# Kernel tuning notes

Hardware: AMD Instinct MI355X
Metric: run time of the kernel (lower is better)

Reference implementation:

```python
import jax, jax.numpy as jnp
import numpy as np


def setup_inputs() -> dict:
    key = jax.random.key(0)
    ks = jax.random.split(key, 7)
    B, L, D, H = 256, 1024, 768, 768
    x = jax.random.normal(ks[0], (B, L, D), dtype=jnp.float32)
    label_mask = jax.random.randint(ks[1], (B, L), 0, 2).astype(jnp.int32)
    global_prototype_tensor = jax.random.normal(ks[2], (L + 1, D), dtype=jnp.float32)
    W_h = jax.random.normal(ks[3], (H, D), dtype=jnp.float32) * 0.02
    b_h = jax.random.normal(ks[4], (H,), dtype=jnp.float32) * 0.02
    W_p = jax.random.normal(ks[5], (D, H), dtype=jnp.float32) * 0.02
    b_p = jax.random.normal(ks[6], (D,), dtype=jnp.float32) * 0.02
    return {"x": x, "label_mask": label_mask,
            "global_prototype_tensor": global_prototype_tensor,
            "W_h": W_h, "b_h": b_h, "W_p": W_p, "b_p": b_p}


def _mlp(v, W_h, b_h, W_p, b_p):
    # torch Linear: y = v @ W.T + b
    h = jax.nn.relu(jnp.einsum('ld,hd->lh', v, W_h) + b_h)
    return jnp.einsum('lh,dh->ld', h, W_p) + b_p


def reference(x, label_mask, global_prototype_tensor, W_h, b_h, W_p, b_p):
    # x: [B, L, D]; label_mask: [B, L] (1 if label i in example's label_list)
    m = label_mask.astype(x.dtype)                        # [B, L]
    pos_cnt = m.sum(0)                                    # [L]
    B = x.shape[0]
    anti_cnt = B - pos_cnt                                # [L]
    pos_sum = jnp.einsum('bl,bld->ld', m, x)              # masked segment-sum
    tot_sum = x.sum(0)                                    # [L, D]
    anti_sum = tot_sum - pos_sum

    pos_mean = pos_sum / jnp.maximum(pos_cnt, 1.0)[:, None]
    anti_mean = anti_sum / jnp.maximum(anti_cnt, 1.0)[:, None]

    avg_pos = 0.5 * pos_mean + 0.5 * global_prototype_tensor[:-1]   # [L, D]
    avg_anti = 0.5 * anti_mean + 0.5 * global_prototype_tensor[-1]  # [L, D]

    proto = _mlp(avg_pos, W_h, b_h, W_p, b_p)
    proto = jnp.where((pos_cnt > 0)[:, None], proto, 0.0)           # rows stay zero if no members

    anti_proto = _mlp(avg_anti, W_h, b_h, W_p, b_p)
    w = (anti_cnt > 0).astype(x.dtype)                              # [L]
    anti = jnp.einsum('l,ld->d', w, anti_proto) / jnp.maximum(w.sum(), 1.0)

    return jnp.concatenate([proto, anti[None, :]], axis=0)          # [L+1, D]
```

## Files before the change

### kernel.cpp

```cpp
#include <hip/hip_runtime.h>

#define L_DIM 1024
#define B_DIM 256
#define D_DIM 768
#define K_DIM 768
#define NTILES (K_DIM / 32)
#define WN    (768 * 768)

typedef _Float16 half8 __attribute__((ext_vector_type(8)));
typedef float    floatx4 __attribute__((ext_vector_type(4)));

__device__ __forceinline__ ushort f2h(float f) {
    _Float16 h = (_Float16)f;
    return __builtin_bit_cast(ushort, h);
}
__device__ __forceinline__ float h2f(ushort u) {
    return (float)__builtin_bit_cast(_Float16, u);
}

__device__ __forceinline__ void gl16(const ushort* g, ushort* l) {
    __builtin_amdgcn_global_load_lds(
        (const __attribute__((address_space(1))) unsigned int*)g,
        (__attribute__((address_space(3))) unsigned int*)l, 16, 0, 0);
}

__global__ __launch_bounds__(768)
void reduce_and_cast(const float* __restrict__ x,
                     const int* __restrict__ mask,
                     const float* __restrict__ gpt,
                     const float* __restrict__ Wh, const float* __restrict__ Wp,
                     ushort* __restrict__ Vhi, ushort* __restrict__ Vlo,
                     ushort* __restrict__ WhH, ushort* __restrict__ WpH,
                     float* __restrict__ pos_cnt, unsigned* __restrict__ counter)
{
    const int tid = threadIdx.x;

    if (blockIdx.x >= 256) {
        const int idx = ((blockIdx.x - 256) * 768 + tid) * 4;
        const float4 v = (idx < WN) ? *(const float4*)(Wh + idx)
                                    : *(const float4*)(Wp + (idx - WN));
        ushort4 o;
        o.x = f2h(v.x); o.y = f2h(v.y); o.z = f2h(v.z); o.w = f2h(v.w);
        if (idx < WN) *(ushort4*)(WhH + idx) = o;
        else          *(ushort4*)(WpH + (idx - WN)) = o;
        return;
    }

    if (blockIdx.x == 0 && tid == 0) *counter = 0u;

    __shared__ int mS[256][4];
    const int l0 = blockIdx.x * 4;
    if (tid < 256)
        *(int4*)&mS[tid][0] = *(const int4*)(mask + (size_t)tid * L_DIM + l0);
    __syncthreads();

    const int row = tid / 192;
    const int t   = tid % 192;
    const int d0  = t * 4;
    const int l   = l0 + row;

    const size_t bstride = (size_t)L_DIM * D_DIM;
    const float* xp = x + (size_t)l * D_DIM + d0;

    floatx4 pos = {0.f, 0.f, 0.f, 0.f};
    floatx4 tot = {0.f, 0.f, 0.f, 0.f};
    float cnt = 0.f;

    #pragma unroll 16
    for (int b = 0; b < B_DIM; ++b) {
        const floatx4 v = __builtin_nontemporal_load((const floatx4*)(xp + (size_t)b * bstride));
        const float fm = (float)mS[b][row];
        tot += v;
        pos[0] = fmaf(fm, v[0], pos[0]);
        pos[1] = fmaf(fm, v[1], pos[1]);
        pos[2] = fmaf(fm, v[2], pos[2]);
        pos[3] = fmaf(fm, v[3], pos[3]);
        cnt += fm;
    }

    const float inv_p = 0.5f / fmaxf(cnt, 1.0f);
    const float inv_a = 0.5f / fmaxf((float)B_DIM - cnt, 1.0f);

    const float4 g4  = *(const float4*)(gpt + (size_t)l * D_DIM + d0);
    const float4 gl4 = *(const float4*)(gpt + (size_t)L_DIM * D_DIM + d0);

    float vp[4], va[4];
    vp[0] = pos[0] * inv_p + 0.5f * g4.x;
    vp[1] = pos[1] * inv_p + 0.5f * g4.y;
    vp[2] = pos[2] * inv_p + 0.5f * g4.z;
    vp[3] = pos[3] * inv_p + 0.5f * g4.w;
    va[0] = (tot[0] - pos[0]) * inv_a + 0.5f * gl4.x;
    va[1] = (tot[1] - pos[1]) * inv_a + 0.5f * gl4.y;
    va[2] = (tot[2] - pos[2]) * inv_a + 0.5f * gl4.z;
    va[3] = (tot[3] - pos[3]) * inv_a + 0.5f * gl4.w;

    ushort4 ph, pl, ah, al;
    ph.x = f2h(vp[0]); pl.x = f2h(vp[0] - h2f(ph.x));
    ph.y = f2h(vp[1]); pl.y = f2h(vp[1] - h2f(ph.y));
    ph.z = f2h(vp[2]); pl.z = f2h(vp[2] - h2f(ph.z));
    ph.w = f2h(vp[3]); pl.w = f2h(vp[3] - h2f(ph.w));
    ah.x = f2h(va[0]); al.x = f2h(va[0] - h2f(ah.x));
    ah.y = f2h(va[1]); al.y = f2h(va[1] - h2f(ah.y));
    ah.z = f2h(va[2]); al.z = f2h(va[2] - h2f(ah.z));
    ah.w = f2h(va[3]); al.w = f2h(va[3] - h2f(ah.w));

    const size_t r0 = (size_t)l * D_DIM + d0;
    const size_t r1 = (size_t)(L_DIM + l) * D_DIM + d0;
    *(ushort4*)(Vhi + r0) = ph;  *(ushort4*)(Vlo + r0) = pl;
    *(ushort4*)(Vhi + r1) = ah;  *(ushort4*)(Vlo + r1) = al;

    if (t == 0) pos_cnt[l] = cnt;
}

template<int MODE>
__global__ __launch_bounds__(256)
void gemm_split(const ushort* __restrict__ Ahi, const ushort* __restrict__ Alo,
                const ushort* __restrict__ Bh, const float* __restrict__ bias,
                ushort* __restrict__ OutHi, ushort* __restrict__ OutLo,
                float* __restrict__ OutF, float* __restrict__ Partial,
                const float* __restrict__ cnt, unsigned* __restrict__ counter)
{
    __shared__ ushort lds[2][8192];
    __shared__ float  colsum[4][64];
    __shared__ float  red[256];
    __shared__ unsigned lastflag;

    const int tid  = threadIdx.x;
    const int lane = tid & 63;
    const int wid  = tid >> 6;
    const int brow = blockIdx.y * 64;
    const int bcol = blockIdx.x * 128;
    const int wr   = (wid >> 1) * 32;
    const int wc   = (wid & 1) * 64;

    const int srow = tid >> 2;
    const int slot = tid & 3;
    const int sk   = (slot ^ ((srow >> 1) & 3)) * 8;

    const ushort* pAh = Ahi + (size_t)(brow + srow) * K_DIM + sk;
    const ushort* pAl = Alo + (size_t)(brow + srow) * K_DIM + sk;
    const ushort* pB0 = Bh  + (size_t)(bcol + srow) * K_DIM + sk;
    const ushort* pB1 = Bh  + (size_t)(bcol + 64 + srow) * K_DIM + sk;

    const int ldst = tid * 8;

    const int q  = lane >> 4;
    const int rA = wr + (lane & 15);
    const int rB = wc + (lane & 15);
    const int fA = rA * 32 + ((q ^ ((rA >> 1) & 3)) << 3);
    const int fB = 4096 + rB * 32 + ((q ^ ((rB >> 1) & 3)) << 3);

    floatx4 acc[2][4] = {};

    gl16(pAh, &lds[0][ldst]);
    gl16(pAl, &lds[0][2048 + ldst]);
    gl16(pB0, &lds[0][4096 + ldst]);
    gl16(pB1, &lds[0][6144 + ldst]);
    __syncthreads();

    for (int t = 0; t < NTILES; ++t) {
        const int cur = t & 1;
        if (t + 1 < NTILES) {
            const int ko = (t + 1) * 32;
            const int nxt = cur ^ 1;
            gl16(pAh + ko, &lds[nxt][ldst]);
            gl16(pAl + ko, &lds[nxt][2048 + ldst]);
            gl16(pB0 + ko, &lds[nxt][4096 + ldst]);
            gl16(pB1 + ko, &lds[nxt][6144 + ldst]);
        }
        half8 ah0 = *(half8*)&lds[cur][fA];
        half8 ah1 = *(half8*)&lds[cur][fA + 512];
        half8 al0 = *(half8*)&lds[cur][2048 + fA];
        half8 al1 = *(half8*)&lds[cur][2048 + fA + 512];
        half8 b0  = *(half8*)&lds[cur][fB];
        half8 b1  = *(half8*)&lds[cur][fB + 512];
        half8 b2  = *(half8*)&lds[cur][fB + 1024];
        half8 b3  = *(half8*)&lds[cur][fB + 1536];

        acc[0][0] = __builtin_amdgcn_mfma_f32_16x16x32_f16(ah0, b0, acc[0][0], 0, 0, 0);
        acc[0][1] = __builtin_amdgcn_mfma_f32_16x16x32_f16(ah0, b1, acc[0][1], 0, 0, 0);
        acc[0][2] = __builtin_amdgcn_mfma_f32_16x16x32_f16(ah0, b2, acc[0][2], 0, 0, 0);
        acc[0][3] = __builtin_amdgcn_mfma_f32_16x16x32_f16(ah0, b3, acc[0][3], 0, 0, 0);
        acc[1][0] = __builtin_amdgcn_mfma_f32_16x16x32_f16(ah1, b0, acc[1][0], 0, 0, 0);
        acc[1][1] = __builtin_amdgcn_mfma_f32_16x16x32_f16(ah1, b1, acc[1][1], 0, 0, 0);
        acc[1][2] = __builtin_amdgcn_mfma_f32_16x16x32_f16(ah1, b2, acc[1][2], 0, 0, 0);
        acc[1][3] = __builtin_amdgcn_mfma_f32_16x16x32_f16(ah1, b3, acc[1][3], 0, 0, 0);
        acc[0][0] = __builtin_amdgcn_mfma_f32_16x16x32_f16(al0, b0, acc[0][0], 0, 0, 0);
        acc[0][1] = __builtin_amdgcn_mfma_f32_16x16x32_f16(al0, b1, acc[0][1], 0, 0, 0);
        acc[0][2] = __builtin_amdgcn_mfma_f32_16x16x32_f16(al0, b2, acc[0][2], 0, 0, 0);
        acc[0][3] = __builtin_amdgcn_mfma_f32_16x16x32_f16(al0, b3, acc[0][3], 0, 0, 0);
        acc[1][0] = __builtin_amdgcn_mfma_f32_16x16x32_f16(al1, b0, acc[1][0], 0, 0, 0);
        acc[1][1] = __builtin_amdgcn_mfma_f32_16x16x32_f16(al1, b1, acc[1][1], 0, 0, 0);
        acc[1][2] = __builtin_amdgcn_mfma_f32_16x16x32_f16(al1, b2, acc[1][2], 0, 0, 0);
        acc[1][3] = __builtin_amdgcn_mfma_f32_16x16x32_f16(al1, b3, acc[1][3], 0, 0, 0);

        __syncthreads();
    }

    if (MODE == 0 || brow < L_DIM) {
        #pragma unroll
        for (int mi = 0; mi < 2; ++mi) {
            #pragma unroll
            for (int ni = 0; ni < 4; ++ni) {
                const int col   = bcol + wc + ni * 16 + (lane & 15);
                const int rbase = brow + wr + mi * 16 + (q << 2);
                const float bv = bias[col];
                #pragma unroll
                for (int r = 0; r < 4; ++r) {
                    const float v = acc[mi][ni][r] + bv;
                    const int row = rbase + r;
                    if (MODE == 0) {
                        const float h = fmaxf(v, 0.f);
                        const ushort hh = f2h(h);
                        OutHi[(size_t)row * D_DIM + col] = hh;
                        OutLo[(size_t)row * D_DIM + col] = f2h(h - h2f(hh));
                    } else {
                        OutF[(size_t)row * D_DIM + col] = (cnt[row] > 0.f) ? v : 0.f;
                    }
                }
            }
        }
    } else {
        float s[4] = {0.f, 0.f, 0.f, 0.f};
        #pragma unroll
        for (int mi = 0; mi < 2; ++mi) {
            const int rbase = brow + wr + mi * 16 + (q << 2);
            #pragma unroll
            for (int r = 0; r < 4; ++r) {
                const float w = (cnt[rbase + r - L_DIM] < 255.5f) ? 1.0f : 0.0f;
                #pragma unroll
                for (int ni = 0; ni < 4; ++ni) {
                    const int col = bcol + wc + ni * 16 + (lane & 15);
                    s[ni] = fmaf(w, acc[mi][ni][r] + bias[col], s[ni]);
                }
            }
        }
        #pragma unroll
        for (int ni = 0; ni < 4; ++ni) {
            s[ni] += __shfl_down(s[ni], 32);
            s[ni] += __shfl_down(s[ni], 16);
            if (lane < 16) colsum[wid][ni * 16 + lane] = s[ni];
        }
        __syncthreads();
        if (tid < 128) {
            const float v = (tid < 64)
                ? colsum[0][tid] + colsum[2][tid]
                : colsum[1][tid - 64] + colsum[3][tid - 64];
            Partial[(size_t)(blockIdx.y - 16) * D_DIM + bcol + tid] = v;
        }
        __threadfence();
        __syncthreads();
        if (tid == 0) lastflag = (atomicAdd(counter, 1u) == 95u) ? 1u : 0u;
        __syncthreads();
        if (lastflag) {
            __threadfence();
            float w = 0.f;
            for (int i = tid; i < L_DIM; i += 256)
                w += (cnt[i] < 255.5f) ? 1.0f : 0.0f;
            red[tid] = w;
            __syncthreads();
            for (int st = 128; st > 0; st >>= 1) {
                if (tid < st) red[tid] += red[tid + st];
                __syncthreads();
            }
            const float wsum = fmaxf(red[0], 1.0f);
            #pragma unroll
            for (int j = 0; j < 3; ++j) {
                const int d = tid + j * 256;
                float sm = 0.f;
                #pragma unroll
                for (int pp = 0; pp < 16; ++pp)
                    sm += Partial[(size_t)pp * D_DIM + d];
                OutF[(size_t)L_DIM * D_DIM + d] = sm / wsum;
            }
        }
    }
}

extern "C" void kernel_launch(void* const* d_in, const int* in_sizes, int n_in,
                              void* d_out, int out_size, void* d_ws, size_t ws_size,
                              hipStream_t stream) {
    const float* x    = (const float*)d_in[0];
    const int*   mask = (const int*)d_in[1];
    const float* gpt  = (const float*)d_in[2];
    const float* W_h  = (const float*)d_in[3];
    const float* b_h  = (const float*)d_in[4];
    const float* W_p  = (const float*)d_in[5];
    const float* b_p  = (const float*)d_in[6];
    float* out = (float*)d_out;

    char* p = (char*)d_ws;
    ushort* Vhi  = (ushort*)p; p += (size_t)2 * L_DIM * D_DIM * 2;
    ushort* Vlo  = (ushort*)p; p += (size_t)2 * L_DIM * D_DIM * 2;
    ushort* Hhi  = (ushort*)p; p += (size_t)2 * L_DIM * D_DIM * 2;
    ushort* Hlo  = (ushort*)p; p += (size_t)2 * L_DIM * D_DIM * 2;
    ushort* WhH  = (ushort*)p; p += (size_t)WN * 2;
    ushort* WpH  = (ushort*)p; p += (size_t)WN * 2;
    float*  Part = (float*)p;  p += (size_t)16 * D_DIM * 4;
    float*  cnt  = (float*)p;  p += (size_t)L_DIM * 4;
    unsigned* counter = (unsigned*)p;

    reduce_and_cast<<<640, 768, 0, stream>>>(x, mask, gpt, W_h, W_p,
                                             Vhi, Vlo, WhH, WpH, cnt, counter);

    dim3 ggrid(D_DIM / 128, 2 * L_DIM / 64);
    gemm_split<0><<<ggrid, 256, 0, stream>>>(Vhi, Vlo, WhH, b_h,
                                             Hhi, Hlo, nullptr, nullptr, nullptr, nullptr);
    gemm_split<1><<<ggrid, 256, 0, stream>>>(Hhi, Hlo, WpH, b_p,
                                             nullptr, nullptr, out, Part, cnt, counter);
}
```

Measured before the change: 184.4 us.

## Drop hi/lo fp16 split for activations and enlarge GEMM row tile to 128

New measurement: 176.9 us (median of 2 runs). 4.1% less time.

```diff
diff --git a/kernel.cpp b/kernel.cpp
--- a/kernel.cpp
+++ b/kernel.cpp
@@ -14,9 +14,6 @@
     _Float16 h = (_Float16)f;
     return __builtin_bit_cast(ushort, h);
 }
-__device__ __forceinline__ float h2f(ushort u) {
-    return (float)__builtin_bit_cast(_Float16, u);
-}
 
 __device__ __forceinline__ void gl16(const ushort* g, ushort* l) {
     __builtin_amdgcn_global_load_lds(
@@ -29,7 +26,7 @@
                      const int* __restrict__ mask,
                      const float* __restrict__ gpt,
                      const float* __restrict__ Wh, const float* __restrict__ Wp,
-                     ushort* __restrict__ Vhi, ushort* __restrict__ Vlo,
+                     ushort* __restrict__ Vh,
                      ushort* __restrict__ WhH, ushort* __restrict__ WpH,
                      float* __restrict__ pos_cnt, unsigned* __restrict__ counter)
 {
@@ -84,41 +81,29 @@
     const float4 g4  = *(const float4*)(gpt + (size_t)l * D_DIM + d0);
     const float4 gl4 = *(const float4*)(gpt + (size_t)L_DIM * D_DIM + d0);
 
-    float vp[4], va[4];
-    vp[0] = pos[0] * inv_p + 0.5f * g4.x;
-    vp[1] = pos[1] * inv_p + 0.5f * g4.y;
-    vp[2] = pos[2] * inv_p + 0.5f * g4.z;
-    vp[3] = pos[3] * inv_p + 0.5f * g4.w;
-    va[0] = (tot[0] - pos[0]) * inv_a + 0.5f * gl4.x;
-    va[1] = (tot[1] - pos[1]) * inv_a + 0.5f * gl4.y;
-    va[2] = (tot[2] - pos[2]) * inv_a + 0.5f * gl4.z;
-    va[3] = (tot[3] - pos[3]) * inv_a + 0.5f * gl4.w;
-
-    ushort4 ph, pl, ah, al;
-    ph.x = f2h(vp[0]); pl.x = f2h(vp[0] - h2f(ph.x));
-    ph.y = f2h(vp[1]); pl.y = f2h(vp[1] - h2f(ph.y));
-    ph.z = f2h(vp[2]); pl.z = f2h(vp[2] - h2f(ph.z));
-    ph.w = f2h(vp[3]); pl.w = f2h(vp[3] - h2f(ph.w));
-    ah.x = f2h(va[0]); al.x = f2h(va[0] - h2f(ah.x));
-    ah.y = f2h(va[1]); al.y = f2h(va[1] - h2f(ah.y));
-    ah.z = f2h(va[2]); al.z = f2h(va[2] - h2f(ah.z));
-    ah.w = f2h(va[3]); al.w = f2h(va[3] - h2f(ah.w));
-
-    const size_t r0 = (size_t)l * D_DIM + d0;
-    const size_t r1 = (size_t)(L_DIM + l) * D_DIM + d0;
-    *(ushort4*)(Vhi + r0) = ph;  *(ushort4*)(Vlo + r0) = pl;
-    *(ushort4*)(Vhi + r1) = ah;  *(ushort4*)(Vlo + r1) = al;
+    ushort4 ph, ah;
+    ph.x = f2h(pos[0] * inv_p + 0.5f * g4.x);
+    ph.y = f2h(pos[1] * inv_p + 0.5f * g4.y);
+    ph.z = f2h(pos[2] * inv_p + 0.5f * g4.z);
+    ph.w = f2h(pos[3] * inv_p + 0.5f * g4.w);
+    ah.x = f2h((tot[0] - pos[0]) * inv_a + 0.5f * gl4.x);
+    ah.y = f2h((tot[1] - pos[1]) * inv_a + 0.5f * gl4.y);
+    ah.z = f2h((tot[2] - pos[2]) * inv_a + 0.5f * gl4.z);
+    ah.w = f2h((tot[3] - pos[3]) * inv_a + 0.5f * gl4.w);
+
+    *(ushort4*)(Vh + (size_t)l * D_DIM + d0) = ph;
+    *(ushort4*)(Vh + (size_t)(L_DIM + l) * D_DIM + d0) = ah;
 
     if (t == 0) pos_cnt[l] = cnt;
 }
 
 template<int MODE>
 __global__ __launch_bounds__(256)
-void gemm_split(const ushort* __restrict__ Ahi, const ushort* __restrict__ Alo,
-                const ushort* __restrict__ Bh, const float* __restrict__ bias,
-                ushort* __restrict__ OutHi, ushort* __restrict__ OutLo,
-                float* __restrict__ OutF, float* __restrict__ Partial,
-                const float* __restrict__ cnt, unsigned* __restrict__ counter)
+void gemm_f16(const ushort* __restrict__ A, const ushort* __restrict__ B,
+              const float* __restrict__ bias,
+              ushort* __restrict__ OutH, float* __restrict__ OutF,
+              float* __restrict__ Partial,
+              const float* __restrict__ cnt, unsigned* __restrict__ counter)
 {
     __shared__ ushort lds[2][8192];
     __shared__ float  colsum[4][64];
@@ -128,32 +113,32 @@
     const int tid  = threadIdx.x;
     const int lane = tid & 63;
     const int wid  = tid >> 6;
-    const int brow = blockIdx.y * 64;
+    const int brow = blockIdx.y * 128;
     const int bcol = blockIdx.x * 128;
-    const int wr   = (wid >> 1) * 32;
+    const int wr   = (wid >> 1) * 64;
     const int wc   = (wid & 1) * 64;
 
     const int srow = tid >> 2;
     const int slot = tid & 3;
     const int sk   = (slot ^ ((srow >> 1) & 3)) * 8;
 
-    const ushort* pAh = Ahi + (size_t)(brow + srow) * K_DIM + sk;
-    const ushort* pAl = Alo + (size_t)(brow + srow) * K_DIM + sk;
-    const ushort* pB0 = Bh  + (size_t)(bcol + srow) * K_DIM + sk;
-    const ushort* pB1 = Bh  + (size_t)(bcol + 64 + srow) * K_DIM + sk;
+    const ushort* pA0 = A + (size_t)(brow + srow) * K_DIM + sk;
+    const ushort* pA1 = A + (size_t)(brow + 64 + srow) * K_DIM + sk;
+    const ushort* pB0 = B + (size_t)(bcol + srow) * K_DIM + sk;
+    const ushort* pB1 = B + (size_t)(bcol + 64 + srow) * K_DIM + sk;
 
     const int ldst = tid * 8;
 
-    const int q  = lane >> 4;
-    const int rA = wr + (lane & 15);
-    const int rB = wc + (lane & 15);
-    const int fA = rA * 32 + ((q ^ ((rA >> 1) & 3)) << 3);
-    const int fB = 4096 + rB * 32 + ((q ^ ((rB >> 1) & 3)) << 3);
-
-    floatx4 acc[2][4] = {};
-
-    gl16(pAh, &lds[0][ldst]);
-    gl16(pAl, &lds[0][2048 + ldst]);
+    const int q   = lane >> 4;
+    const int r15 = lane & 15;
+    const int swz = ((q ^ ((r15 >> 1) & 3)) << 3);
+    const int fA  = (wr + r15) * 32 + swz;
+    const int fB  = 4096 + (wc + r15) * 32 + swz;
+
+    floatx4 acc[4][4] = {};
+
+    gl16(pA0, &lds[0][ldst]);
+    gl16(pA1, &lds[0][2048 + ldst]);
     gl16(pB0, &lds[0][4096 + ldst]);
     gl16(pB1, &lds[0][6144 + ldst]);
     __syncthreads();
@@ -163,46 +148,31 @@
         if (t + 1 < NTILES) {
             const int ko = (t + 1) * 32;
             const int nxt = cur ^ 1;
-            gl16(pAh + ko, &lds[nxt][ldst]);
-            gl16(pAl + ko, &lds[nxt][2048 + ldst]);
+            gl16(pA0 + ko, &lds[nxt][ldst]);
+            gl16(pA1 + ko, &lds[nxt][2048 + ldst]);
             gl16(pB0 + ko, &lds[nxt][4096 + ldst]);
             gl16(pB1 + ko, &lds[nxt][6144 + ldst]);
         }
-        half8 ah0 = *(half8*)&lds[cur][fA];
-        half8 ah1 = *(half8*)&lds[cur][fA + 512];
-        half8 al0 = *(half8*)&lds[cur][2048 + fA];
-        half8 al1 = *(half8*)&lds[cur][2048 + fA + 512];
-        half8 b0  = *(half8*)&lds[cur][fB];
-        half8 b1  = *(half8*)&lds[cur][fB + 512];
-        half8 b2  = *(half8*)&lds[cur][fB + 1024];
-        half8 b3  = *(half8*)&lds[cur][fB + 1536];
-
-        acc[0][0] = __builtin_amdgcn_mfma_f32_16x16x32_f16(ah0, b0, acc[0][0], 0, 0, 0);
-        acc[0][1] = __builtin_amdgcn_mfma_f32_16x16x32_f16(ah0, b1, acc[0][1], 0, 0, 0);
-        acc[0][2] = __builtin_amdgcn_mfma_f32_16x16x32_f16(ah0, b2, acc[0][2], 0, 0, 0);
-        acc[0][3] = __builtin_amdgcn_mfma_f32_16x16x32_f16(ah0, b3, acc[0][3], 0, 0, 0);
-        acc[1][0] = __builtin_amdgcn_mfma_f32_16x16x32_f16(ah1, b0, acc[1][0], 0, 0, 0);
-        acc[1][1] = __builtin_amdgcn_mfma_f32_16x16x32_f16(ah1, b1, acc[1][1], 0, 0, 0);
-        acc[1][2] = __builtin_amdgcn_mfma_f32_16x16x32_f16(ah1, b2, acc[1][2], 0, 0, 0);
-        acc[1][3] = __builtin_amdgcn_mfma_f32_16x16x32_f16(ah1, b3, acc[1][3], 0, 0, 0);
-        acc[0][0] = __builtin_amdgcn_mfma_f32_16x16x32_f16(al0, b0, acc[0][0], 0, 0, 0);
-        acc[0][1] = __builtin_amdgcn_mfma_f32_16x16x32_f16(al0, b1, acc[0][1], 0, 0, 0);
-        acc[0][2] = __builtin_amdgcn_mfma_f32_16x16x32_f16(al0, b2, acc[0][2], 0, 0, 0);
-        acc[0][3] = __builtin_amdgcn_mfma_f32_16x16x32_f16(al0, b3, acc[0][3], 0, 0, 0);
-        acc[1][0] = __builtin_amdgcn_mfma_f32_16x16x32_f16(al1, b0, acc[1][0], 0, 0, 0);
-        acc[1][1] = __builtin_amdgcn_mfma_f32_16x16x32_f16(al1, b1, acc[1][1], 0, 0, 0);
-        acc[1][2] = __builtin_amdgcn_mfma_f32_16x16x32_f16(al1, b2, acc[1][2], 0, 0, 0);
-        acc[1][3] = __builtin_amdgcn_mfma_f32_16x16x32_f16(al1, b3, acc[1][3], 0, 0, 0);
-
+        half8 a[4], b[4];
+        #pragma unroll
+        for (int i = 0; i < 4; ++i) {
+            a[i] = *(half8*)&lds[cur][fA + i * 512];
+            b[i] = *(half8*)&lds[cur][fB + i * 512];
+        }
+        #pragma unroll
+        for (int mi = 0; mi < 4; ++mi)
+            #pragma unroll
+            for (int ni = 0; ni < 4; ++ni)
+                acc[mi][ni] = __builtin_amdgcn_mfma_f32_16x16x32_f16(a[mi], b[ni], acc[mi][ni], 0, 0, 0);
         __syncthreads();
     }
 
     if (MODE == 0 || brow < L_DIM) {
         #pragma unroll
-        for (int mi = 0; mi < 2; ++mi) {
+        for (int mi = 0; mi < 4; ++mi) {
             #pragma unroll
             for (int ni = 0; ni < 4; ++ni) {
-                const int col   = bcol + wc + ni * 16 + (lane & 15);
+                const int col   = bcol + wc + ni * 16 + r15;
                 const int rbase = brow + wr + mi * 16 + (q << 2);
                 const float bv = bias[col];
                 #pragma unroll
@@ -210,10 +180,7 @@
                     const float v = acc[mi][ni][r] + bv;
                     const int row = rbase + r;
                     if (MODE == 0) {
-                        const float h = fmaxf(v, 0.f);
-                        const ushort hh = f2h(h);
-                        OutHi[(size_t)row * D_DIM + col] = hh;
-                        OutLo[(size_t)row * D_DIM + col] = f2h(h - h2f(hh));
+                        OutH[(size_t)row * D_DIM + col] = f2h(fmaxf(v, 0.f));
                     } else {
                         OutF[(size_t)row * D_DIM + col] = (cnt[row] > 0.f) ? v : 0.f;
                     }
@@ -223,14 +190,14 @@
     } else {
         float s[4] = {0.f, 0.f, 0.f, 0.f};
         #pragma unroll
-        for (int mi = 0; mi < 2; ++mi) {
+        for (int mi = 0; mi < 4; ++mi) {
             const int rbase = brow + wr + mi * 16 + (q << 2);
             #pragma unroll
             for (int r = 0; r < 4; ++r) {
                 const float w = (cnt[rbase + r - L_DIM] < 255.5f) ? 1.0f : 0.0f;
                 #pragma unroll
                 for (int ni = 0; ni < 4; ++ni) {
-                    const int col = bcol + wc + ni * 16 + (lane & 15);
+                    const int col = bcol + wc + ni * 16 + r15;
                     s[ni] = fmaf(w, acc[mi][ni][r] + bias[col], s[ni]);
                 }
             }
@@ -246,11 +213,11 @@
             const float v = (tid < 64)
                 ? colsum[0][tid] + colsum[2][tid]
                 : colsum[1][tid - 64] + colsum[3][tid - 64];
-            Partial[(size_t)(blockIdx.y - 16) * D_DIM + bcol + tid] = v;
+            Partial[(size_t)(blockIdx.y - 8) * D_DIM + bcol + tid] = v;
         }
         __threadfence();
         __syncthreads();
-        if (tid == 0) lastflag = (atomicAdd(counter, 1u) == 95u) ? 1u : 0u;
+        if (tid == 0) lastflag = (atomicAdd(counter, 1u) == 47u) ? 1u : 0u;
         __syncthreads();
         if (lastflag) {
             __threadfence();
@@ -269,7 +236,7 @@
                 const int d = tid + j * 256;
                 float sm = 0.f;
                 #pragma unroll
-                for (int pp = 0; pp < 16; ++pp)
+                for (int pp = 0; pp < 8; ++pp)
                     sm += Partial[(size_t)pp * D_DIM + d];
                 OutF[(size_t)L_DIM * D_DIM + d] = sm / wsum;
             }
@@ -290,22 +257,20 @@
     float* out = (float*)d_out;
 
     char* p = (char*)d_ws;
-    ushort* Vhi  = (ushort*)p; p += (size_t)2 * L_DIM * D_DIM * 2;
-    ushort* Vlo  = (ushort*)p; p += (size_t)2 * L_DIM * D_DIM * 2;
-    ushort* Hhi  = (ushort*)p; p += (size_t)2 * L_DIM * D_DIM * 2;
-    ushort* Hlo  = (ushort*)p; p += (size_t)2 * L_DIM * D_DIM * 2;
+    ushort* Vh   = (ushort*)p; p += (size_t)2 * L_DIM * D_DIM * 2;
+    ushort* Hh   = (ushort*)p; p += (size_t)2 * L_DIM * D_DIM * 2;
     ushort* WhH  = (ushort*)p; p += (size_t)WN * 2;
     ushort* WpH  = (ushort*)p; p += (size_t)WN * 2;
-    float*  Part = (float*)p;  p += (size_t)16 * D_DIM * 4;
+    float*  Part = (float*)p;  p += (size_t)8 * D_DIM * 4;
     float*  cnt  = (float*)p;  p += (size_t)L_DIM * 4;
     unsigned* counter = (unsigned*)p;
 
     reduce_and_cast<<<640, 768, 0, stream>>>(x, mask, gpt, W_h, W_p,
-                                             Vhi, Vlo, WhH, WpH, cnt, counter);
-
-    dim3 ggrid(D_DIM / 128, 2 * L_DIM / 64);
-    gemm_split<0><<<ggrid, 256, 0, stream>>>(Vhi, Vlo, WhH, b_h,
-                                             Hhi, Hlo, nullptr, nullptr, nullptr, nullptr);
-    gemm_split<1><<<ggrid, 256, 0, stream>>>(Hhi, Hlo, WpH, b_p,
-                                             nullptr, nullptr, out, Part, cnt, counter);
-}
+                                             Vh, WhH, WpH, cnt, counter);
+
+    dim3 ggrid(D_DIM / 128, 2 * L_DIM / 128);
+    gemm_f16<0><<<ggrid, 256, 0, stream>>>(Vh, WhH, b_h,
+                                           Hh, nullptr, nullptr, nullptr, nullptr);
+    gemm_f16<1><<<ggrid, 256, 0, stream>>>(Hh, WpH, b_p,
+                                           nullptr, out, Part, cnt, counter);
+}
```
